# Kernel tuning notes

Measured on AMD Instinct MI355X. Metric: run time of the kernel, lower is better.

The kernel has to match this reference:

```python
import jax, jax.numpy as jnp
import numpy as np

U, I, B, E = 256, 1024, 512, 64


def setup_inputs() -> dict:
    key = jax.random.key(0)
    k1, k2, k3, k4, k5 = jax.random.split(key, 5)
    # Dense stand-in for self.sparse_tensor: [num_users, num_items, num_items]
    T = jax.random.normal(k1, (U, I, I), dtype=jnp.float32) * 0.05
    gu = jax.random.normal(k2, (B, E), dtype=jnp.float32)
    gi = jax.random.normal(k3, (B, E), dtype=jnp.float32)
    users = jax.random.randint(k4, (B,), 0, U)
    items = jax.random.randint(k5, (B,), 0, I)
    return {"T": T, "gu": gu, "gi": gi, "users": users, "items": items}


def reference(T, gu, gi, users, items):
    # forward2: sparse[b, m, k] = T[users[b], items[m], items[k]]
    # gamma_i_i[b] = sum_{m,k} sparse[b,m,k] * gi[k]
    # Fused form: gather rows, reduce over m, gather cols, single GEMM with gi.
    g1 = T[users[:, None], items[None, :], :]      # [B, B, I] gathered slabs
    row_sum = jnp.sum(g1, axis=1)                  # [B, I] sum over m (items rows)
    sel = row_sum[:, items]                        # [B, B] select item columns
    gamma_i_i = sel @ gi                           # [B, E]
    # torch.nn.functional.normalize(p=2, dim=1), eps=1e-12
    norm = jnp.linalg.norm(gamma_i_i, axis=1, keepdims=True)
    gamma_i_i = gamma_i_i / jnp.maximum(norm, 1e-12)
    gamma_u = gu                                   # squeeze is a no-op on [B, E]
    xui = jnp.sum(gamma_u * gamma_i_i, axis=1)     # [B]
    return (xui, gamma_u, gamma_i_i)
```

## Files before the change

### kernel.cpp

```cpp
#include <hip/hip_runtime.h>
#include <hip/hip_bf16.h>


#define U_CNT 256
#define I_CNT 1024
#define B_CNT 512
#define E_CNT 64
#define CMAX  528

__global__ __launch_bounds__(1024) void setup_kernel(
    const int* __restrict__ users, const int* __restrict__ items,
    int* __restrict__ citems, float* __restrict__ ccnts,
    int* __restrict__ meta, int* __restrict__ upresent) {
  __shared__ int cnt[I_CNT];
  __shared__ int dcount;
  int tid = threadIdx.x;
  cnt[tid] = 0;
  if (tid == 0) dcount = 0;
  if (tid < U_CNT) upresent[tid] = 0;
  __syncthreads();
  if (tid < B_CNT) atomicAdd(&cnt[items[tid]], 1);
  __syncthreads();
  if (tid < B_CNT) upresent[users[tid]] = 1;
  int c = cnt[tid];
  if (c > 0) {
    int pos = atomicAdd(&dcount, 1);
    citems[pos] = tid;
    ccnts[pos]  = (float)c;
  }
  __syncthreads();
  int D = dcount;
  int Dpad = (D + 7) & ~7;
  if (tid >= D && tid < Dpad) { citems[tid] = 0; ccnts[tid] = 0.0f; }
  if (tid == 0) meta[0] = Dpad;
}

__global__ __launch_bounds__(256) void rowsum_kernel(
    const float* __restrict__ T, const int* __restrict__ citems,
    const float* __restrict__ ccnts, const int* __restrict__ meta,
    const int* __restrict__ upresent, float* __restrict__ rs) {
  int u    = blockIdx.x >> 1;
  int half = blockIdx.x & 1;
  if (!upresent[u]) return;

  __shared__ int   s_items[CMAX];
  __shared__ float s_cnts[CMAX];
  int Dpad = meta[0];
  for (int i = threadIdx.x; i < Dpad; i += 256) {
    s_items[i] = citems[i];
    s_cnts[i]  = ccnts[i];
  }
  __syncthreads();

  const float2* Tu = (const float2*)(T + ((size_t)u << 20));
  int col2 = half * 256 + threadIdx.x;
  float2 acc = make_float2(0.0f, 0.0f);

  for (int d = 0; d < Dpad; d += 8) {
    int   idx[8];
    float cf[8];
#pragma unroll
    for (int k = 0; k < 8; ++k) { idx[k] = s_items[d + k]; cf[k] = s_cnts[d + k]; }
    float2 t[8];
#pragma unroll
    for (int k = 0; k < 8; ++k) t[k] = Tu[(size_t)idx[k] * 512 + col2];
#pragma unroll
    for (int k = 0; k < 8; ++k) {
      acc.x = fmaf(cf[k], t[k].x, acc.x);
      acc.y = fmaf(cf[k], t[k].y, acc.y);
    }
  }
  ((float2*)(rs + ((size_t)u << 10)))[col2] = acc;
}

__global__ __launch_bounds__(256) void gamma_kernel(
    const float* __restrict__ rs, const float* __restrict__ gi,
    const int* __restrict__ items, const int* __restrict__ upresent,
    float* __restrict__ vn) {
  int u = blockIdx.x;
  if (!upresent[u]) return;

  __shared__ float w[B_CNT];
  __shared__ float partial[4][E_CNT];
  int tid = threadIdx.x;
  const float* rsu = rs + ((size_t)u << 10);
  for (int j = tid; j < B_CNT; j += 256) w[j] = rsu[items[j]];
  __syncthreads();

  int e = tid & 63, q = tid >> 6;
  float acc = 0.0f;
  int j0 = q * 128;
#pragma unroll 4
  for (int j = j0; j < j0 + 128; ++j) acc = fmaf(w[j], gi[j * E_CNT + e], acc);
  partial[q][e] = acc;
  __syncthreads();

  if (q == 0) {
    float v = partial[0][e] + partial[1][e] + partial[2][e] + partial[3][e];
    float sq = v * v;
    for (int off = 32; off > 0; off >>= 1) sq += __shfl_down(sq, off);
    float n = __shfl(sq, 0);
    n = fmaxf(sqrtf(n), 1e-12f);
    vn[((size_t)u << 6) + e] = v / n;
  }
}

__global__ __launch_bounds__(64) void out_kernel(
    const float* __restrict__ gu, const int* __restrict__ users,
    const float* __restrict__ vn, float* __restrict__ out) {
  int b = blockIdx.x;
  int e = threadIdx.x;
  int u = users[b];
  float g  = gu[b * E_CNT + e];
  float vi = vn[((size_t)u << 6) + e];
  out[B_CNT + b * E_CNT + e] = g;
  out[B_CNT + B_CNT * E_CNT + b * E_CNT + e] = vi;
  float p = g * vi;
  for (int off = 32; off > 0; off >>= 1) p += __shfl_down(p, off);
  if (e == 0) out[b] = p;
}

extern "C" void kernel_launch(void* const* d_in, const int* in_sizes, int n_in,
                              void* d_out, int out_size, void* d_ws, size_t ws_size,
                              hipStream_t stream) {
  const float* T     = (const float*)d_in[0];
  const float* gu    = (const float*)d_in[1];
  const float* gi    = (const float*)d_in[2];
  const int*   users = (const int*)d_in[3];
  const int*   items = (const int*)d_in[4];
  float* out = (float*)d_out;

  float* rs   = (float*)d_ws;
  float* vn   = rs + U_CNT * I_CNT;
  int*   citems = (int*)(vn + U_CNT * E_CNT);
  float* ccnts  = (float*)(citems + CMAX);
  int*   meta   = (int*)(ccnts + CMAX);
  int*   upres  = meta + 8;

  hipLaunchKernelGGL(setup_kernel, dim3(1), dim3(1024), 0, stream,
                     users, items, citems, ccnts, meta, upres);
  hipLaunchKernelGGL(rowsum_kernel, dim3(2 * U_CNT), dim3(256), 0, stream,
                     T, citems, ccnts, meta, upres, rs);
  hipLaunchKernelGGL(gamma_kernel, dim3(U_CNT), dim3(256), 0, stream,
                     rs, gi, items, upres, vn);
  hipLaunchKernelGGL(out_kernel, dim3(B_CNT), dim3(64), 0, stream,
                     gu, users, vn, out);
}
```

Before: 1.217 ms.

## Compact present users, split rowsum over item halves with float4 loads, fuse output kernel

The setup kernel now builds a compacted list of the distinct users so that rowsum and gamma blocks are assigned to present users instead of all 256 user slots. Rowsum splits each user's distinct-item rows between two blocks, each loading full 1024-wide rows with float4, and writes two partial row sums that the gamma kernel adds. The separate output kernel is merged into the gamma kernel, which scans the batch for matching users and writes the outputs, saving one launch. The cost is an extra partial-sum buffer and a serial scan over 512 batch entries in every gamma block.

```diff
diff --git a/kernel.cpp b/kernel.cpp
--- a/kernel.cpp
+++ b/kernel.cpp
@@ -11,37 +11,45 @@
 __global__ __launch_bounds__(1024) void setup_kernel(
     const int* __restrict__ users, const int* __restrict__ items,
     int* __restrict__ citems, float* __restrict__ ccnts,
-    int* __restrict__ meta, int* __restrict__ upresent) {
+    int* __restrict__ cusers, int* __restrict__ meta) {
   __shared__ int cnt[I_CNT];
-  __shared__ int dcount;
+  __shared__ int ucnt[U_CNT];
+  __shared__ int dcount, ucount;
   int tid = threadIdx.x;
   cnt[tid] = 0;
-  if (tid == 0) dcount = 0;
-  if (tid < U_CNT) upresent[tid] = 0;
+  if (tid < U_CNT) ucnt[tid] = 0;
+  if (tid == 0) { dcount = 0; ucount = 0; }
   __syncthreads();
-  if (tid < B_CNT) atomicAdd(&cnt[items[tid]], 1);
+  if (tid < B_CNT) {
+    atomicAdd(&cnt[items[tid]], 1);
+    atomicAdd(&ucnt[users[tid]], 1);
+  }
   __syncthreads();
-  if (tid < B_CNT) upresent[users[tid]] = 1;
   int c = cnt[tid];
   if (c > 0) {
     int pos = atomicAdd(&dcount, 1);
     citems[pos] = tid;
     ccnts[pos]  = (float)c;
   }
+  if (tid < U_CNT && ucnt[tid] > 0) {
+    int pos = atomicAdd(&ucount, 1);
+    cusers[pos] = tid;
+  }
   __syncthreads();
   int D = dcount;
-  int Dpad = (D + 7) & ~7;
+  int Dpad = (D + 15) & ~15;
   if (tid >= D && tid < Dpad) { citems[tid] = 0; ccnts[tid] = 0.0f; }
-  if (tid == 0) meta[0] = Dpad;
+  if (tid == 0) { meta[0] = Dpad; meta[1] = ucount; }
 }
 
 __global__ __launch_bounds__(256) void rowsum_kernel(
     const float* __restrict__ T, const int* __restrict__ citems,
-    const float* __restrict__ ccnts, const int* __restrict__ meta,
-    const int* __restrict__ upresent, float* __restrict__ rs) {
-  int u    = blockIdx.x >> 1;
+    const float* __restrict__ ccnts, const int* __restrict__ cusers,
+    const int* __restrict__ meta, float* __restrict__ rs2) {
+  int w    = blockIdx.x >> 1;
   int half = blockIdx.x & 1;
-  if (!upresent[u]) return;
+  if (w >= meta[1]) return;
+  int u = cusers[w];
 
   __shared__ int   s_items[CMAX];
   __shared__ float s_cnts[CMAX];
@@ -52,46 +60,60 @@
   }
   __syncthreads();
 
-  const float2* Tu = (const float2*)(T + ((size_t)u << 20));
-  int col2 = half * 256 + threadIdx.x;
-  float2 acc = make_float2(0.0f, 0.0f);
+  int Dh = Dpad >> 1;
+  const float4* Tu4 = (const float4*)(T + ((size_t)u << 20));
+  int tid = threadIdx.x;
+  float4 acc = make_float4(0.0f, 0.0f, 0.0f, 0.0f);
 
-  for (int d = 0; d < Dpad; d += 8) {
+  int d0 = half * Dh;
+  for (int d = d0; d < d0 + Dh; d += 8) {
     int   idx[8];
     float cf[8];
 #pragma unroll
     for (int k = 0; k < 8; ++k) { idx[k] = s_items[d + k]; cf[k] = s_cnts[d + k]; }
-    float2 t[8];
+    float4 t[8];
 #pragma unroll
-    for (int k = 0; k < 8; ++k) t[k] = Tu[(size_t)idx[k] * 512 + col2];
+    for (int k = 0; k < 8; ++k) t[k] = Tu4[(size_t)idx[k] * 256 + tid];
 #pragma unroll
     for (int k = 0; k < 8; ++k) {
       acc.x = fmaf(cf[k], t[k].x, acc.x);
       acc.y = fmaf(cf[k], t[k].y, acc.y);
+      acc.z = fmaf(cf[k], t[k].z, acc.z);
+      acc.w = fmaf(cf[k], t[k].w, acc.w);
     }
   }
-  ((float2*)(rs + ((size_t)u << 10)))[col2] = acc;
+  float4* dst = (float4*)(rs2 + ((size_t)(half * U_CNT + u) << 10));
+  dst[tid] = acc;
 }
 
-__global__ __launch_bounds__(256) void gamma_kernel(
-    const float* __restrict__ rs, const float* __restrict__ gi,
-    const int* __restrict__ items, const int* __restrict__ upresent,
-    float* __restrict__ vn) {
-  int u = blockIdx.x;
-  if (!upresent[u]) return;
+__global__ __launch_bounds__(256) void gamma_out_kernel(
+    const float* __restrict__ rs2, const float* __restrict__ gi,
+    const int* __restrict__ items, const int* __restrict__ users,
+    const int* __restrict__ cusers, const int* __restrict__ meta,
+    const float* __restrict__ gu, float* __restrict__ out) {
+  int w = blockIdx.x;
+  if (w >= meta[1]) return;
+  int u = cusers[w];
 
-  __shared__ float w[B_CNT];
+  __shared__ float wgt[B_CNT];
+  __shared__ int   s_users[B_CNT];
   __shared__ float partial[4][E_CNT];
+  __shared__ float vsh[E_CNT];
   int tid = threadIdx.x;
-  const float* rsu = rs + ((size_t)u << 10);
-  for (int j = tid; j < B_CNT; j += 256) w[j] = rsu[items[j]];
+  const float* rsA = rs2 + ((size_t)u << 10);
+  const float* rsB = rs2 + ((size_t)(U_CNT + u) << 10);
+  for (int j = tid; j < B_CNT; j += 256) {
+    int it = items[j];
+    wgt[j]     = rsA[it] + rsB[it];
+    s_users[j] = users[j];
+  }
   __syncthreads();
 
   int e = tid & 63, q = tid >> 6;
   float acc = 0.0f;
   int j0 = q * 128;
 #pragma unroll 4
-  for (int j = j0; j < j0 + 128; ++j) acc = fmaf(w[j], gi[j * E_CNT + e], acc);
+  for (int j = j0; j < j0 + 128; ++j) acc = fmaf(wgt[j], gi[j * E_CNT + e], acc);
   partial[q][e] = acc;
   __syncthreads();
 
@@ -101,23 +123,22 @@
     for (int off = 32; off > 0; off >>= 1) sq += __shfl_down(sq, off);
     float n = __shfl(sq, 0);
     n = fmaxf(sqrtf(n), 1e-12f);
-    vn[((size_t)u << 6) + e] = v / n;
+    vsh[e] = v / n;
   }
-}
+  __syncthreads();
 
-__global__ __launch_bounds__(64) void out_kernel(
-    const float* __restrict__ gu, const int* __restrict__ users,
-    const float* __restrict__ vn, float* __restrict__ out) {
-  int b = blockIdx.x;
-  int e = threadIdx.x;
-  int u = users[b];
-  float g  = gu[b * E_CNT + e];
-  float vi = vn[((size_t)u << 6) + e];
-  out[B_CNT + b * E_CNT + e] = g;
-  out[B_CNT + B_CNT * E_CNT + b * E_CNT + e] = vi;
-  float p = g * vi;
-  for (int off = 32; off > 0; off >>= 1) p += __shfl_down(p, off);
-  if (e == 0) out[b] = p;
+  float vi = vsh[e];
+  int b0 = q * 128;
+  for (int b = b0; b < b0 + 128; ++b) {
+    if (s_users[b] == u) {
+      float g = gu[b * E_CNT + e];
+      out[B_CNT + b * E_CNT + e] = g;
+      out[B_CNT + B_CNT * E_CNT + b * E_CNT + e] = vi;
+      float p = g * vi;
+      for (int off = 32; off > 0; off >>= 1) p += __shfl_down(p, off);
+      if (e == 0) out[b] = p;
+    }
+  }
 }
 
 extern "C" void kernel_launch(void* const* d_in, const int* in_sizes, int n_in,
@@ -130,19 +151,16 @@
   const int*   items = (const int*)d_in[4];
   float* out = (float*)d_out;
 
-  float* rs   = (float*)d_ws;
-  float* vn   = rs + U_CNT * I_CNT;
-  int*   citems = (int*)(vn + U_CNT * E_CNT);
+  float* rs2    = (float*)d_ws;
+  int*   citems = (int*)(rs2 + 2 * U_CNT * I_CNT);
   float* ccnts  = (float*)(citems + CMAX);
-  int*   meta   = (int*)(ccnts + CMAX);
-  int*   upres  = meta + 8;
+  int*   cusers = (int*)(ccnts + CMAX);
+  int*   meta   = cusers + U_CNT;
 
   hipLaunchKernelGGL(setup_kernel, dim3(1), dim3(1024), 0, stream,
-                     users, items, citems, ccnts, meta, upres);
+                     users, items, citems, ccnts, cusers, meta);
   hipLaunchKernelGGL(rowsum_kernel, dim3(2 * U_CNT), dim3(256), 0, stream,
-                     T, citems, ccnts, meta, upres, rs);
-  hipLaunchKernelGGL(gamma_kernel, dim3(U_CNT), dim3(256), 0, stream,
-                     rs, gi, items, upres, vn);
-  hipLaunchKernelGGL(out_kernel, dim3(B_CNT), dim3(64), 0, stream,
-                     gu, users, vn, out);
+                     T, citems, ccnts, cusers, meta, rs2);
+  hipLaunchKernelGGL(gamma_out_kernel, dim3(U_CNT), dim3(256), 0, stream,
+                     rs2, gi, items, users, cusers, meta, gu, out);
 }
```

Result: no change. 1.224 ms (+0.6%).
